# Kernel optimization log

Measured on AMD Instinct MI355X. Metric: run time of the kernel, lower is better.

Reference implementation:

```python
import jax, jax.numpy as jnp
import numpy as np

IN_FEATURES = 4096
OUT_FEATURES = 4096
ROWS_PER_BLOCK = OUT_FEATURES // 2  # two (d, n) config blocks of rows
D = 2  # codeword dimension for both blocks


def setup_inputs() -> dict:
    key = jax.random.key(0)
    ks = jax.random.split(key, 6)
    x = jax.random.normal(ks[0], (2, 2048, IN_FEATURES), dtype=jnp.float32)
    codes_2_256 = jax.random.randint(ks[1], (ROWS_PER_BLOCK, IN_FEATURES // D), 0, 256, dtype=jnp.int32)
    codes_2_16 = jax.random.randint(ks[2], (ROWS_PER_BLOCK, IN_FEATURES // D), 0, 16, dtype=jnp.int32)
    grid_2_256 = jax.random.normal(ks[3], (256, D), dtype=jnp.float32)
    grid_2_16 = jax.random.normal(ks[4], (16, D), dtype=jnp.float32)
    scales = jax.random.uniform(ks[5], (OUT_FEATURES,), dtype=jnp.float32, minval=0.5, maxval=1.5)
    bias = jax.random.normal(jax.random.fold_in(key, 7), (OUT_FEATURES,), dtype=jnp.float32)
    return {
        "x": x,
        "codes_2_256": codes_2_256,
        "codes_2_16": codes_2_16,
        "grid_2_256": grid_2_256,
        "grid_2_16": grid_2_16,
        "scales": scales,
        "bias": bias,
    }


def _dequant_block(codes, grid, rows):
    # codes: [rows, in/d] int -> grid lookup [rows, in/d, d] -> [rows, in]
    return grid[codes].reshape(rows, IN_FEATURES)


def reference(x, codes_2_256, codes_2_16, grid_2_256, grid_2_16, scales, bias):
    # Reconstruct weight blocks from per-group VQ codebooks (HIGGS dequant).
    w_top = _dequant_block(codes_2_256, grid_2_256, ROWS_PER_BLOCK)    # [2048, 4096]
    w_bot = _dequant_block(codes_2_16, grid_2_16, ROWS_PER_BLOCK)      # [2048, 4096]
    weight = jnp.concatenate([w_top, w_bot], axis=0) * scales[:, None]  # [out, in]
    # y = x @ W^T + b  (F.linear)
    y = jnp.einsum("bsi,oi->bso", x, weight) + bias
    return y
```

## Files before the change

kernel.cpp:

```cpp
#include <hip/hip_runtime.h>
#include <hip/hip_fp16.h>


#define M_TOK 4096
#define K_DIM 4096
#define N_DIM 4096

typedef _Float16 half8 __attribute__((ext_vector_type(8)));
typedef float floatx4 __attribute__((ext_vector_type(4)));

__global__ void dequant_w(const int* __restrict__ c256, const int* __restrict__ c16,
                          const float* __restrict__ g256, const float* __restrict__ g16,
                          const float* __restrict__ scales,
                          _Float16* __restrict__ Wh)
{
    int idx = blockIdx.x * blockDim.x + threadIdx.x;
    int row = idx >> 9;
    float s = scales[row];
    int4 cd;
    const float* g;
    if (row < 2048) { cd = ((const int4*)c256)[idx]; g = g256; }
    else            { cd = ((const int4*)c16)[idx - (2048*2048/4)]; g = g16; }
    union U { _Float16 h[8]; ulong2 u; } w;
    w.h[0] = (_Float16)(g[2*cd.x]   * s);
    w.h[1] = (_Float16)(g[2*cd.x+1] * s);
    w.h[2] = (_Float16)(g[2*cd.y]   * s);
    w.h[3] = (_Float16)(g[2*cd.y+1] * s);
    w.h[4] = (_Float16)(g[2*cd.z]   * s);
    w.h[5] = (_Float16)(g[2*cd.z+1] * s);
    w.h[6] = (_Float16)(g[2*cd.w]   * s);
    w.h[7] = (_Float16)(g[2*cd.w+1] * s);
    ((ulong2*)Wh)[idx] = w.u;
}

__global__ void cast_x(const float* __restrict__ x, _Float16* __restrict__ xh)
{
    int idx = blockIdx.x * blockDim.x + threadIdx.x;
    float4 v0 = ((const float4*)x)[2*idx];
    float4 v1 = ((const float4*)x)[2*idx + 1];
    union U { _Float16 h[8]; ulong2 u; } o;
    o.h[0] = (_Float16)v0.x; o.h[1] = (_Float16)v0.y;
    o.h[2] = (_Float16)v0.z; o.h[3] = (_Float16)v0.w;
    o.h[4] = (_Float16)v1.x; o.h[5] = (_Float16)v1.y;
    o.h[6] = (_Float16)v1.z; o.h[7] = (_Float16)v1.w;
    ((ulong2*)xh)[idx] = o.u;
}

#define BM 128
#define BN 128
#define BK 32

__device__ __forceinline__ void gl2lds16(const void* g, void* l)
{
    __builtin_amdgcn_global_load_lds(
        (const __attribute__((address_space(1))) void*)g,
        (__attribute__((address_space(3))) void*)l, 16, 0, 0);
}

__global__ __launch_bounds__(256)
void gemm1(const _Float16* __restrict__ Xh, const _Float16* __restrict__ Wh,
           const float* __restrict__ bias, float* __restrict__ C)
{
    __shared__ _Float16 As[BM * BK];
    __shared__ _Float16 Bs[BN * BK];

    const int orig = blockIdx.x;
    const int wgid = (orig & 7) * 128 + (orig >> 3);
    const int bx   = wgid & 31;
    const int by   = wgid >> 5;

    const int t    = threadIdx.x;
    const int lane = t & 63;
    const int wave = t >> 6;
    const int wr   = wave >> 1;
    const int wc   = wave & 1;
    const int brow = by * BM;
    const int bcol = bx * BN;

    const int lrow = lane & 15;
    const int lk   = (lane >> 4) * 8;

    const int srow = t >> 2;
    const int sk   = (t & 3) * 8;

    floatx4 acc[4][4];
    #pragma unroll
    for (int m = 0; m < 4; ++m)
        #pragma unroll
        for (int n = 0; n < 4; ++n)
            #pragma unroll
            for (int r = 0; r < 4; ++r) acc[m][n][r] = 0.0f;

    const _Float16* Ag = Xh + (size_t)brow * K_DIM;
    const _Float16* Bg = Wh + (size_t)bcol * K_DIM;

    for (int kt = 0; kt < K_DIM; kt += BK) {
        __syncthreads();
        #pragma unroll
        for (int j = 0; j < 2; ++j) {
            const size_t go = (size_t)(j*64 + srow) * K_DIM + kt + sk;
            const int    lo = j*2048 + t*8;
            gl2lds16(Ag + go, &As[lo]);
            gl2lds16(Bg + go, &Bs[lo]);
        }
        __syncthreads();

        half8 a[4], b[4];
        #pragma unroll
        for (int m = 0; m < 4; ++m)
            a[m] = *(const half8*)&As[(wr*64 + m*16 + lrow) * BK + lk];
        #pragma unroll
        for (int n = 0; n < 4; ++n)
            b[n] = *(const half8*)&Bs[(wc*64 + n*16 + lrow) * BK + lk];

        #pragma unroll
        for (int m = 0; m < 4; ++m)
            #pragma unroll
            for (int n = 0; n < 4; ++n)
                acc[m][n] = __builtin_amdgcn_mfma_f32_16x16x32_f16(
                                a[m], b[n], acc[m][n], 0, 0, 0);
    }

    #pragma unroll
    for (int n = 0; n < 4; ++n) {
        const int col = bcol + wc*64 + n*16 + lrow;
        const float bv = bias[col];
        #pragma unroll
        for (int m = 0; m < 4; ++m) {
            const int rbase = brow + wr*64 + m*16 + (lane >> 4) * 4;
            #pragma unroll
            for (int r = 0; r < 4; ++r)
                C[(size_t)(rbase + r) * N_DIM + col] = acc[m][n][r] + bv;
        }
    }
}

extern "C" void kernel_launch(void* const* d_in, const int* in_sizes, int n_in,
                              void* d_out, int out_size, void* d_ws, size_t ws_size,
                              hipStream_t stream)
{
    const float* x      = (const float*)d_in[0];
    const int*   c256   = (const int*)  d_in[1];
    const int*   c16    = (const int*)  d_in[2];
    const float* g256   = (const float*)d_in[3];
    const float* g16    = (const float*)d_in[4];
    const float* scales = (const float*)d_in[5];
    const float* bias   = (const float*)d_in[6];
    float*       out    = (float*)d_out;

    char* ws = (char*)d_ws;
    const size_t SZ = (size_t)K_DIM * N_DIM * sizeof(_Float16);
    _Float16* Wh = (_Float16*)(ws + 0*SZ);
    _Float16* Xh = (_Float16*)(ws + 1*SZ);

    dequant_w<<<dim3((4096*2048/4)/256), dim3(256), 0, stream>>>(
        c256, c16, g256, g16, scales, Wh);
    cast_x<<<dim3((M_TOK*K_DIM/8)/256), dim3(256), 0, stream>>>(x, Xh);
    gemm1<<<dim3(1024), dim3(256), 0, stream>>>(Xh, Wh, bias, out);
}
```

Before: 346.8 us.

## Replace GEMM with 256x256-tile, 8-wave, double-buffered LDS pipelined kernel

```diff
diff --git a/kernel.cpp b/kernel.cpp
--- a/kernel.cpp
+++ b/kernel.cpp
@@ -5,6 +5,7 @@
 #define M_TOK 4096
 #define K_DIM 4096
 #define N_DIM 4096
+#define NT    (K_DIM / 64)
 
 typedef _Float16 half8 __attribute__((ext_vector_type(8)));
 typedef float floatx4 __attribute__((ext_vector_type(4)));
@@ -46,10 +47,6 @@
     ((ulong2*)xh)[idx] = o.u;
 }
 
-#define BM 128
-#define BN 128
-#define BK 32
-
 __device__ __forceinline__ void gl2lds16(const void* g, void* l)
 {
     __builtin_amdgcn_global_load_lds(
@@ -57,68 +54,105 @@
         (__attribute__((address_space(3))) void*)l, 16, 0, 0);
 }
 
-__global__ __launch_bounds__(256)
-void gemm1(const _Float16* __restrict__ Xh, const _Float16* __restrict__ Wh,
-           const float* __restrict__ bias, float* __restrict__ C)
+#define STAGE(buf, unit, pan, kcol)                                          \
+    { _Float16* lb = &lds[(buf)*32768 + (unit)*8192];                        \
+      gl2lds16((pan) + goff0 + (kcol), lb + t*8);                            \
+      gl2lds16((pan) + goff1 + (kcol), lb + (512+t)*8); }
+
+#define RD_A(q, mm) (*(const half8*)&lds[cur*32768 + ((q)>>1)*2*8192 +       \
+      ((wr*8 + ((q)&1)*4 + (mm))*64 + kbr*16 + lrow)*8])
+#define RD_B(q, n)  (*(const half8*)&lds[cur*32768 + (((q)>>1)*2+1)*8192 +   \
+      ((wc*4 + (n))*64 + kbr*16 + lrow)*8])
+
+#define PHASE_MFMA(q)                                                        \
+    __builtin_amdgcn_s_setprio(1);                                           \
+    _Pragma("unroll")                                                        \
+    for (int mm = 0; mm < 4; ++mm) {                                         \
+        _Pragma("unroll")                                                    \
+        for (int n = 0; n < 4; ++n)                                          \
+            acc[((q)&1)*4+mm][n] = __builtin_amdgcn_mfma_f32_16x16x32_f16(   \
+                a[mm], b[n], acc[((q)&1)*4+mm][n], 0, 0, 0);                 \
+    }                                                                        \
+    __builtin_amdgcn_s_setprio(0);
+
+#define BOUNDARY(morev)                                                      \
+    if (morev) asm volatile("s_waitcnt vmcnt(4)" ::: "memory");              \
+    else       asm volatile("s_waitcnt vmcnt(0)" ::: "memory");              \
+    __builtin_amdgcn_s_barrier();                                            \
+    asm volatile("" ::: "memory");
+
+__global__ __launch_bounds__(512, 2)
+void gemm8p(const _Float16* __restrict__ Xh, const _Float16* __restrict__ Wh,
+            const float* __restrict__ bias, float* __restrict__ C)
 {
-    __shared__ _Float16 As[BM * BK];
-    __shared__ _Float16 Bs[BN * BK];
-
-    const int orig = blockIdx.x;
-    const int wgid = (orig & 7) * 128 + (orig >> 3);
-    const int bx   = wgid & 31;
-    const int by   = wgid >> 5;
+    extern __shared__ _Float16 lds[];
 
     const int t    = threadIdx.x;
     const int lane = t & 63;
-    const int wave = t >> 6;
-    const int wr   = wave >> 1;
-    const int wc   = wave & 1;
-    const int brow = by * BM;
-    const int bcol = bx * BN;
+    const int w    = t >> 6;
+    const int wr   = w >> 2;
+    const int wc   = w & 3;
+    const int lrow = lane & 15;
+    const int kbr  = lane >> 4;
 
-    const int lrow = lane & 15;
-    const int lk   = (lane >> 4) * 8;
+    const int swz  = (blockIdx.x & 7) * 32 + (blockIdx.x >> 3);
+    const int bx   = swz & 15;
+    const int by   = swz >> 4;
+    const int brow = by * 256;
+    const int bcol = bx * 256;
 
-    const int srow = t >> 2;
-    const int sk   = (t & 3) * 8;
+    const int idx0 = t,        idx1 = 512 + t;
+    const size_t goff0 = (size_t)((idx0 >> 6)*16 + (idx0 & 15)) * K_DIM + ((idx0 >> 4) & 3)*8;
+    const size_t goff1 = (size_t)((idx1 >> 6)*16 + (idx1 & 15)) * K_DIM + ((idx1 >> 4) & 3)*8;
 
-    floatx4 acc[4][4];
+    const _Float16* Apan = Xh + (size_t)brow * K_DIM;
+    const _Float16* Bpan = Wh + (size_t)bcol * K_DIM;
+
+    floatx4 acc[8][4];
     #pragma unroll
-    for (int m = 0; m < 4; ++m)
+    for (int m = 0; m < 8; ++m)
         #pragma unroll
         for (int n = 0; n < 4; ++n)
             #pragma unroll
             for (int r = 0; r < 4; ++r) acc[m][n][r] = 0.0f;
 
-    const _Float16* Ag = Xh + (size_t)brow * K_DIM;
-    const _Float16* Bg = Wh + (size_t)bcol * K_DIM;
+    STAGE(0, 0, Apan, 0);
+    STAGE(0, 1, Bpan, 0);
+    STAGE(0, 2, Apan, 32);
+    STAGE(0, 3, Bpan, 32);
 
-    for (int kt = 0; kt < K_DIM; kt += BK) {
-        __syncthreads();
+    for (int tau = 0; tau < NT; ++tau) {
+        const int  cur  = tau & 1;
+        const int  nxt  = cur ^ 1;
+        const int  kn   = (tau + 1) * 64;
+        const bool more = (tau + 1 < NT);
+        half8 a[4], b[4];
+
+        BOUNDARY(more);
         #pragma unroll
-        for (int j = 0; j < 2; ++j) {
-            const size_t go = (size_t)(j*64 + srow) * K_DIM + kt + sk;
-            const int    lo = j*2048 + t*8;
-            gl2lds16(Ag + go, &As[lo]);
-            gl2lds16(Bg + go, &Bs[lo]);
-        }
-        __syncthreads();
-
-        half8 a[4], b[4];
+        for (int n = 0; n < 4; ++n)  b[n] = RD_B(0, n);
         #pragma unroll
-        for (int m = 0; m < 4; ++m)
-            a[m] = *(const half8*)&As[(wr*64 + m*16 + lrow) * BK + lk];
-        #pragma unroll
-        for (int n = 0; n < 4; ++n)
-            b[n] = *(const half8*)&Bs[(wc*64 + n*16 + lrow) * BK + lk];
+        for (int mm = 0; mm < 4; ++mm) a[mm] = RD_A(0, mm);
+        if (more) STAGE(nxt, 0, Apan, kn);
+        PHASE_MFMA(0);
 
         #pragma unroll
-        for (int m = 0; m < 4; ++m)
-            #pragma unroll
-            for (int n = 0; n < 4; ++n)
-                acc[m][n] = __builtin_amdgcn_mfma_f32_16x16x32_f16(
-                                a[m], b[n], acc[m][n], 0, 0, 0);
+        for (int mm = 0; mm < 4; ++mm) a[mm] = RD_A(1, mm);
+        if (more) STAGE(nxt, 1, Bpan, kn);
+        PHASE_MFMA(1);
+
+        BOUNDARY(more);
+        #pragma unroll
+        for (int n = 0; n < 4; ++n)  b[n] = RD_B(2, n);
+        #pragma unroll
+        for (int mm = 0; mm < 4; ++mm) a[mm] = RD_A(2, mm);
+        if (more) STAGE(nxt, 2, Apan, kn + 32);
+        PHASE_MFMA(2);
+
+        #pragma unroll
+        for (int mm = 0; mm < 4; ++mm) a[mm] = RD_A(3, mm);
+        if (more) STAGE(nxt, 3, Bpan, kn + 32);
+        PHASE_MFMA(3);
     }
 
     #pragma unroll
@@ -126,8 +160,8 @@
         const int col = bcol + wc*64 + n*16 + lrow;
         const float bv = bias[col];
         #pragma unroll
-        for (int m = 0; m < 4; ++m) {
-            const int rbase = brow + wr*64 + m*16 + (lane >> 4) * 4;
+        for (int m = 0; m < 8; ++m) {
+            const int rbase = brow + wr*128 + m*16 + kbr*4;
             #pragma unroll
             for (int r = 0; r < 4; ++r)
                 C[(size_t)(rbase + r) * N_DIM + col] = acc[m][n][r] + bv;
@@ -153,8 +187,11 @@
     _Float16* Wh = (_Float16*)(ws + 0*SZ);
     _Float16* Xh = (_Float16*)(ws + 1*SZ);
 
+    hipFuncSetAttribute((const void*)gemm8p,
+                        hipFuncAttributeMaxDynamicSharedMemorySize, 131072);
+
     dequant_w<<<dim3((4096*2048/4)/256), dim3(256), 0, stream>>>(
         c256, c16, g256, g16, scales, Wh);
     cast_x<<<dim3((M_TOK*K_DIM/8)/256), dim3(256), 0, stream>>>(x, Xh);
-    gemm1<<<dim3(1024), dim3(256), 0, stream>>>(Xh, Wh, bias, out);
+    gemm8p<<<dim3(256), dim3(512), 131072, stream>>>(Xh, Wh, bias, out);
 }
```

Result: faster. 295.3 us (-14.9%).
